# Optimization experiments

Measured on AMD Instinct MI355X. Metric: run time of the kernel, lower is better.

Reference implementation:

```python
import jax, jax.numpy as jnp
import numpy as np

B, S, DIM, H, D = 2, 2048, 1024, 16, 64
WINDOW = 512
MAX_MEM_SEGMENTS = 1
ROPE_THETA = 10000.0


def _rope(t, pos):
    # lucidrains rotary-embedding-torch default: interleaved pairs
    d = t.shape[-1]
    inv_freq = 1.0 / (ROPE_THETA ** (jnp.arange(0, d, 2, dtype=jnp.float32) / d))
    freqs = pos[:, None].astype(jnp.float32) * inv_freq[None, :]        # [S, d/2]
    freqs = jnp.repeat(freqs, 2, axis=-1)                               # [S, d]
    cos, sin = jnp.cos(freqs), jnp.sin(freqs)
    t1, t2 = t[..., 0::2], t[..., 1::2]
    rot = jnp.stack((-t2, t1), axis=-1).reshape(t.shape)                # rotate_half
    return t * cos + rot * sin


def setup_inputs() -> dict:
    key = jax.random.key(0)
    ks = jax.random.split(key, 8)
    tokens = jax.random.normal(ks[0], (B, S, DIM), dtype=jnp.float32)
    value_residual = jax.random.normal(ks[1], (B, H, S, D), dtype=jnp.float32)
    episode_ids = jnp.sort(jax.random.randint(ks[2], (B, S), 0, 4), axis=-1)
    w = 0.02
    Wq = jax.random.normal(ks[3], (DIM, H * D), dtype=jnp.float32) * w
    Wkv = jax.random.normal(ks[4], (DIM, 2 * H * D), dtype=jnp.float32) * w
    Wo = jax.random.normal(ks[5], (H * D, DIM), dtype=jnp.float32) * w
    Wg = jax.random.normal(ks[6], (DIM, H), dtype=jnp.float32) * w
    Wmix = jax.random.normal(ks[7], (DIM, H), dtype=jnp.float32) * w
    return {"tokens": tokens, "value_residual": value_residual, "episode_ids": episode_ids,
            "Wq": Wq, "Wkv": Wkv, "Wo": Wo, "Wg": Wg, "Wmix": Wmix}


def reference(tokens, value_residual, episode_ids, Wq, Wkv, Wo, Wg, Wmix):
    b, s, _ = tokens.shape
    scale = D ** -0.5

    def split_heads(x):  # [b, n, h*d] -> [b, h, n, d]
        return x.reshape(b, s, H, D).transpose(0, 2, 1, 3)

    q = split_heads(tokens @ Wq)
    kv = tokens @ Wkv
    k, v = split_heads(kv[..., :H * D]), split_heads(kv[..., H * D:])

    q = q * scale

    # value-residual lerp: v.lerp(value_residual, mix)
    mix = jax.nn.sigmoid(jnp.einsum('bnd,dh->bhn', tokens, Wmix))[..., None]  # [b,h,n,1]
    v = v + mix * (value_residual - v)

    pos = jnp.arange(s)
    q = _rope(q, pos)
    k = _rope(k, pos)

    sim = jnp.einsum('bhid,bhjd->bhij', q, k)

    # fixed-window causal mask: masked where dist < 0 or dist > max_mem_segments*window
    dist = pos[:, None] - pos[None, :]
    win_mask = (dist < 0) | (dist > MAX_MEM_SEGMENTS * WINDOW)            # [s, s]
    ep_mask = episode_ids[:, :, None] != episode_ids[:, None, :]          # [b, s, s]
    mask = win_mask[None, None, :, :] | ep_mask[:, None, :, :]

    sim = jnp.where(mask, -jnp.finfo(sim.dtype).max, sim)
    attn = jax.nn.softmax(sim, axis=-1)
    out = jnp.einsum('bhij,bhjd->bhid', attn, v)

    # sigmoid value gating
    gate = jax.nn.sigmoid(jnp.einsum('bnd,dh->bhn', tokens, Wg))[..., None]
    out = out * gate

    out = out.transpose(0, 2, 1, 3).reshape(b, s, H * D)
    return out @ Wo
```

## Files before the change

### kernel.cpp

```cpp
#include <hip/hip_runtime.h>
#include <math.h>

#define BB 2
#define SS 2048
#define DIMM 1024
#define HH 16
#define DD 64
#define WINDOW 512

typedef __bf16 bf16x8 __attribute__((ext_vector_type(8)));
typedef float f32x4 __attribute__((ext_vector_type(4)));

__device__ __forceinline__ unsigned short f2bf(float f) {
    unsigned int u = __float_as_uint(f);
    u = (u + 0x7FFFu + ((u >> 16) & 1u)) >> 16;
    return (unsigned short)u;
}
__device__ __forceinline__ float bf2f(unsigned short u) {
    return __uint_as_float((unsigned int)u << 16);
}

__device__ __forceinline__ void async_cp16(unsigned short* lds_dst, const unsigned short* g_src) {
    __builtin_amdgcn_global_load_lds(
        (const __attribute__((address_space(1))) unsigned int*)g_src,
        (__attribute__((address_space(3))) unsigned int*)lds_dst, 16, 0, 0);
}

__global__ __launch_bounds__(256) void cvt_bf16_kernel(
    const float* __restrict__ src, unsigned short* __restrict__ dst, int n4)
{
    for (int i = blockIdx.x * 256 + threadIdx.x; i < n4; i += gridDim.x * 256) {
        float4 v = ((const float4*)src)[i];
        ushort4 o;
        o.x = f2bf(v.x); o.y = f2bf(v.y); o.z = f2bf(v.z); o.w = f2bf(v.w);
        ((ushort4*)dst)[i] = o;
    }
}

__global__ __launch_bounds__(256) void transpose_cvt_kernel(
    const float* __restrict__ src, unsigned short* __restrict__ dst, int R, int C)
{
    __shared__ float t[32][33];
    int c0 = blockIdx.x * 32, r0 = blockIdx.y * 32;
    int tx = threadIdx.x, ty = threadIdx.y;
    #pragma unroll
    for (int u = 0; u < 4; ++u)
        t[ty + 8 * u][tx] = src[(size_t)(r0 + ty + 8 * u) * C + c0 + tx];
    __syncthreads();
    #pragma unroll
    for (int u = 0; u < 4; ++u)
        dst[(size_t)(c0 + ty + 8 * u) * R + r0 + tx] = f2bf(t[tx][ty + 8 * u]);
}

__global__ __launch_bounds__(256) void build_wgmt_kernel(
    const float* __restrict__ Wg, const float* __restrict__ Wmix,
    unsigned short* __restrict__ dst)
{
    int idx = blockIdx.x * 256 + threadIdx.x;
    int n = idx >> 10, k = idx & 1023;
    const float* src = (n < 16) ? Wg : Wmix;
    dst[idx] = f2bf(src[k * HH + (n & 15)]);
}

__global__ __launch_bounds__(256) void mixgate_mfma(
    const unsigned short* __restrict__ A,
    const unsigned short* __restrict__ Bt,
    float* __restrict__ gate, float* __restrict__ mix)
{
    int mbase = blockIdx.x * 32;
    int tid = threadIdx.x;
    int wave = tid >> 6, lane = tid & 63;
    int fr = lane & 15, hi = lane >> 4;
    int kw = wave * 256;

    __shared__ float red[4][32][32];

    f32x4 acc[2][2];
    #pragma unroll
    for (int m_ = 0; m_ < 2; ++m_)
        #pragma unroll
        for (int n_ = 0; n_ < 2; ++n_)
            acc[m_][n_] = (f32x4){0.f, 0.f, 0.f, 0.f};

    const unsigned short* a0 = A + (size_t)(mbase + fr) * 1024 + kw + hi * 8;
    const unsigned short* a1 = A + (size_t)(mbase + 16 + fr) * 1024 + kw + hi * 8;
    const unsigned short* b0 = Bt + (size_t)fr * 1024 + kw + hi * 8;
    const unsigned short* b1 = Bt + (size_t)(16 + fr) * 1024 + kw + hi * 8;

    #pragma unroll 2
    for (int k = 0; k < 256; k += 32) {
        bf16x8 af0 = *(const bf16x8*)(a0 + k);
        bf16x8 af1 = *(const bf16x8*)(a1 + k);
        bf16x8 bf0 = *(const bf16x8*)(b0 + k);
        bf16x8 bf1 = *(const bf16x8*)(b1 + k);
        acc[0][0] = __builtin_amdgcn_mfma_f32_16x16x32_bf16(af0, bf0, acc[0][0], 0, 0, 0);
        acc[0][1] = __builtin_amdgcn_mfma_f32_16x16x32_bf16(af0, bf1, acc[0][1], 0, 0, 0);
        acc[1][0] = __builtin_amdgcn_mfma_f32_16x16x32_bf16(af1, bf0, acc[1][0], 0, 0, 0);
        acc[1][1] = __builtin_amdgcn_mfma_f32_16x16x32_bf16(af1, bf1, acc[1][1], 0, 0, 0);
    }

    #pragma unroll
    for (int m_ = 0; m_ < 2; ++m_)
        #pragma unroll
        for (int n_ = 0; n_ < 2; ++n_)
            #pragma unroll
            for (int j = 0; j < 4; ++j)
                red[wave][m_ * 16 + hi * 4 + j][n_ * 16 + fr] = acc[m_][n_][j];
    __syncthreads();

    #pragma unroll
    for (int e = 0; e < 4; ++e) {
        int idx = (tid << 2) | e;
        int r = idx >> 5, c = idx & 31;
        float s4 = red[0][r][c] + red[1][r][c] + red[2][r][c] + red[3][r][c];
        float sg = 1.f / (1.f + __expf(-s4));
        int mg = mbase + r;
        int b = mg >> 11, s = mg & 2047;
        int h = c & 15;
        float* dst = (c < 16) ? gate : mix;
        dst[((size_t)b * HH + h) * SS + s] = sg;
    }
}

__global__ __launch_bounds__(256) void epstart_kernel(
    const int* __restrict__ ep, int* __restrict__ epstart)
{
    int idx = blockIdx.x * 256 + threadIdx.x;
    int b = idx >> 11, i = idx & 2047;
    const int* e = ep + b * SS;
    int v = e[i];
    int lo = 0, hi = i;
    while (lo < hi) {
        int mid = (lo + hi) >> 1;
        if (e[mid] == v) hi = mid; else lo = mid + 1;
    }
    epstart[idx] = lo;
}

template<int EPI>
__global__ __launch_bounds__(256) void gemm_mfma(
    const unsigned short* __restrict__ A, const unsigned short* __restrict__ Bt,
    void* __restrict__ o0v, void* __restrict__ o1v, void* __restrict__ o2v)
{
    const int K = 1024;
    int nbase = blockIdx.x * 128;
    int mbase = blockIdx.y * 128;
    int tid = threadIdx.x;
    int lane = tid & 63;
    int wave = tid >> 6;
    int wr = wave >> 1, wc = wave & 1;
    int fr = lane & 15, hi = lane >> 4;

    __shared__ unsigned short As[128 * 32];
    __shared__ unsigned short Bs[128 * 32];

    int srow = tid >> 2;
    int sp   = tid & 3;
    int scol = (sp ^ ((srow >> 1) & 3)) * 8;
    const unsigned short* agp0 = A  + (size_t)(mbase + srow) * K + scol;
    const unsigned short* agp1 = A  + (size_t)(mbase + srow + 64) * K + scol;
    const unsigned short* bgp0 = Bt + (size_t)(nbase + srow) * K + scol;
    const unsigned short* bgp1 = Bt + (size_t)(nbase + srow + 64) * K + scol;
    unsigned short* al0 = &As[tid * 8];
    unsigned short* al1 = &As[2048 + tid * 8];
    unsigned short* bl0 = &Bs[tid * 8];
    unsigned short* bl1 = &Bs[2048 + tid * 8];

    f32x4 acc[4][4];
    #pragma unroll
    for (int m_ = 0; m_ < 4; ++m_)
        #pragma unroll
        for (int n_ = 0; n_ < 4; ++n_)
            acc[m_][n_] = (f32x4){0.f, 0.f, 0.f, 0.f};

    int aidx[4], bidx[4];
    #pragma unroll
    for (int m_ = 0; m_ < 4; ++m_) {
        int row = wr * 64 + m_ * 16 + fr;
        aidx[m_] = row * 32 + (hi ^ ((row >> 1) & 3)) * 8;
    }
    #pragma unroll
    for (int n_ = 0; n_ < 4; ++n_) {
        int row = wc * 64 + n_ * 16 + fr;
        bidx[n_] = row * 32 + (hi ^ ((row >> 1) & 3)) * 8;
    }

    for (int k0 = 0; k0 < K; k0 += 32) {
        __syncthreads();
        async_cp16(al0, agp0 + k0);
        async_cp16(al1, agp1 + k0);
        async_cp16(bl0, bgp0 + k0);
        async_cp16(bl1, bgp1 + k0);
        __syncthreads();

        bf16x8 af[4], bfr[4];
        #pragma unroll
        for (int m_ = 0; m_ < 4; ++m_) af[m_] = *(const bf16x8*)&As[aidx[m_]];
        #pragma unroll
        for (int n_ = 0; n_ < 4; ++n_) bfr[n_] = *(const bf16x8*)&Bs[bidx[n_]];
        #pragma unroll
        for (int m_ = 0; m_ < 4; ++m_)
            #pragma unroll
            for (int n_ = 0; n_ < 4; ++n_)
                acc[m_][n_] = __builtin_amdgcn_mfma_f32_16x16x32_bf16(
                    af[m_], bfr[n_], acc[m_][n_], 0, 0, 0);
    }

    #pragma unroll
    for (int m_ = 0; m_ < 4; ++m_) {
        #pragma unroll
        for (int n_ = 0; n_ < 4; ++n_) {
            int c = nbase + wc * 64 + n_ * 16 + fr;
            #pragma unroll
            for (int j = 0; j < 4; ++j) {
                int mg = mbase + wr * 64 + m_ * 16 + hi * 4 + j;
                float v = acc[m_][n_][j];
                if (EPI == 0) {
                    ((float*)o0v)[(size_t)mg * 1024 + c] = v;
                } else {
                    int b = mg >> 11, s = mg & 2047;
                    int cc = c & 1023, h = cc >> 6, d = cc & 63;
                    unsigned short* dst = (c < 1024) ? (unsigned short*)o0v
                                        : (c < 2048) ? (unsigned short*)o1v
                                                     : (unsigned short*)o2v;
                    dst[(((size_t)b * HH + h) * SS + s) * DD + d] = f2bf(v);
                }
            }
        }
    }
}

__global__ __launch_bounds__(256) void rope_lerp_kernel(
    unsigned short* __restrict__ q, unsigned short* __restrict__ k,
    const unsigned short* __restrict__ v0, const float* __restrict__ vres,
    const float* __restrict__ mix, unsigned short* __restrict__ vt)
{
    int st = blockIdx.x;
    int bh = blockIdx.y;
    int tid = threadIdx.x;
    int sl = tid >> 2;
    int dg = (tid & 3) * 16;
    int s = st * 64 + sl;
    size_t rowoff = ((size_t)bh * SS + s) * DD + dg;

    __shared__ unsigned short vtile[64][66];

    union { uint4 v[2]; unsigned short u[16]; } qa, ka, va;
    qa.v[0] = *(const uint4*)(q + rowoff);
    qa.v[1] = *(const uint4*)(q + rowoff + 8);
    ka.v[0] = *(const uint4*)(k + rowoff);
    ka.v[1] = *(const uint4*)(k + rowoff + 8);
    va.v[0] = *(const uint4*)(v0 + rowoff);
    va.v[1] = *(const uint4*)(v0 + rowoff + 8);
    float4 w[4];
    #pragma unroll
    for (int u = 0; u < 4; ++u) w[u] = *(const float4*)(vres + rowoff + 4 * u);
    float mx = mix[(size_t)bh * SS + s];

    #pragma unroll
    for (int u = 0; u < 8; ++u) {
        int d0 = dg + 2 * u;
        float inv_freq = powf(10000.f, -(float)d0 * (1.f / 64.f));
        float fr = (float)s * inv_freq;
        float red = fr - 6.2831853f * floorf(fr * 0.15915494f);
        float cs, sn;
        __sincosf(red, &sn, &cs);
        float x = bf2f(qa.u[2 * u]), y = bf2f(qa.u[2 * u + 1]);
        qa.u[2 * u]     = f2bf((x * cs - y * sn) * 0.125f);
        qa.u[2 * u + 1] = f2bf((y * cs + x * sn) * 0.125f);
        x = bf2f(ka.u[2 * u]); y = bf2f(ka.u[2 * u + 1]);
        ka.u[2 * u]     = f2bf(x * cs - y * sn);
        ka.u[2 * u + 1] = f2bf(y * cs + x * sn);
    }
    *(uint4*)(q + rowoff)     = qa.v[0];
    *(uint4*)(q + rowoff + 8) = qa.v[1];
    *(uint4*)(k + rowoff)     = ka.v[0];
    *(uint4*)(k + rowoff + 8) = ka.v[1];

    #pragma unroll
    for (int e = 0; e < 16; ++e) {
        float vv = bf2f(va.u[e]);
        float wr = ((const float*)w)[e];
        vtile[sl][dg + e] = f2bf(vv + mx * (wr - vv));
    }
    __syncthreads();

    int d = tid >> 2;
    int sseg = (tid & 3) * 16;
    union { uint4 v[2]; unsigned short u[16]; } ot;
    #pragma unroll
    for (int e = 0; e < 16; ++e) ot.u[e] = vtile[sseg + e][d];
    unsigned short* dst = vt + ((size_t)bh * DD + d) * SS + st * 64 + sseg;
    *(uint4*)dst = ot.v[0];
    *(uint4*)(dst + 8) = ot.v[1];
}

__global__ __launch_bounds__(256) void attn_mfma(
    const unsigned short* __restrict__ qbh, const unsigned short* __restrict__ kbh,
    const unsigned short* __restrict__ vt, const int* __restrict__ epstart,
    const float* __restrict__ gate, unsigned short* __restrict__ ao)
{
    int orig = blockIdx.x;
    int swz  = (orig & 7) * 128 + (orig >> 3);
    int bh = swz >> 5, qt = swz & 31;
    int b = bh >> 4, h = bh & 15;
    int q0 = qt * 64;
    int tid = threadIdx.x;
    int wave = tid >> 6, lane = tid & 63;
    int lq = lane & 15, lg = lane >> 4;
    int i = q0 + wave * 16 + lq;

    __shared__ unsigned short Ks[4096];
    __shared__ unsigned short Vs[4096];
    alignas(16) __shared__ unsigned short P_lds[4][16][72];

    int srow0 = tid >> 3, sch = tid & 7;
    int srow1 = srow0 + 32;
    int sc0 = ((sch ^ (srow0 & 7)) << 3);
    int sc1 = ((sch ^ (srow1 & 7)) << 3);
    const unsigned short* kS0 = kbh + ((size_t)bh * SS + srow0) * DD + sc0;
    const unsigned short* kS1 = kbh + ((size_t)bh * SS + srow1) * DD + sc1;
    const unsigned short* vS0 = vt + ((size_t)bh * DD + srow0) * SS + sc0;
    const unsigned short* vS1 = vt + ((size_t)bh * DD + srow1) * SS + sc1;
    unsigned short* kd0 = &Ks[tid * 8];
    unsigned short* kd1 = &Ks[2048 + tid * 8];
    unsigned short* vd0 = &Vs[tid * 8];
    unsigned short* vd1 = &Vs[2048 + tid * 8];

    int fidx[4];
    #pragma unroll
    for (int n = 0; n < 4; ++n) {
        int r = 16 * n + lq;
        fidx[n] = r * 64 + ((lg ^ (r & 7)) << 3);
    }

    const unsigned short* qrow = qbh + ((size_t)bh * SS + i) * DD + lg * 8;
    bf16x8 bq0 = *(const bf16x8*)qrow;
    bf16x8 bq1 = *(const bf16x8*)(qrow + 32);

    int jmin = i - WINDOW;
    int es = epstart[b * SS + i];
    if (es > jmin) jmin = es;
    float gi = gate[(size_t)bh * SS + i];

    float m = -1e30f, l = 0.f;
    f32x4 o[4];
    #pragma unroll
    for (int n = 0; n < 4; ++n) o[n] = (f32x4){0.f, 0.f, 0.f, 0.f};

    int t0 = (qt < 8) ? (8 - qt) : 0;
    for (int t = t0; t < 9; ++t) {
        int jbase = 64 * (qt - 8 + t);

        __syncthreads();
        async_cp16(kd0, kS0 + (size_t)jbase * DD);
        async_cp16(kd1, kS1 + (size_t)jbase * DD);
        async_cp16(vd0, vS0 + jbase);
        async_cp16(vd1, vS1 + jbase);
        __syncthreads();

        f32x4 acc[4];
        #pragma unroll
        for (int n = 0; n < 4; ++n) acc[n] = (f32x4){0.f, 0.f, 0.f, 0.f};
        #pragma unroll
        for (int n = 0; n < 4; ++n) {
            bf16x8 kf0 = *(const bf16x8*)&Ks[fidx[n]];
            bf16x8 kf1 = *(const bf16x8*)&Ks[fidx[n] ^ 32];
            acc[n] = __builtin_amdgcn_mfma_f32_16x16x32_bf16(kf0, bq0, acc[n], 0, 0, 0);
            acc[n] = __builtin_amdgcn_mfma_f32_16x16x32_bf16(kf1, bq1, acc[n], 0, 0, 0);
        }

        int jb = jbase + lg * 4;
        #pragma unroll
        for (int n = 0; n < 4; ++n)
            #pragma unroll
            for (int r = 0; r < 4; ++r) {
                int j = jb + 16 * n + r;
                if (j < jmin || j > i) acc[n][r] = -3e38f;
            }

        float tm = -3e38f;
        #pragma unroll
        for (int n = 0; n < 4; ++n)
            tm = fmaxf(tm, fmaxf(fmaxf(acc[n][0], acc[n][1]), fmaxf(acc[n][2], acc[n][3])));
        tm = fmaxf(tm, __shfl_xor(tm, 16, 64));
        tm = fmaxf(tm, __shfl_xor(tm, 32, 64));
        float mnew = fmaxf(m, tm);
        float scale = __expf(m - mnew);
        float ts = 0.f;
        #pragma unroll
        for (int n = 0; n < 4; ++n)
            #pragma unroll
            for (int r = 0; r < 4; ++r) {
                float p = __expf(acc[n][r] - mnew);
                acc[n][r] = p;
                ts += p;
            }
        ts += __shfl_xor(ts, 16, 64);
        ts += __shfl_xor(ts, 32, 64);
        l = l * scale + ts;
        m = mnew;
        #pragma unroll
        for (int n = 0; n < 4; ++n) o[n] = o[n] * scale;

        #pragma unroll
        for (int n = 0; n < 4; ++n) {
            ushort4 u;
            u.x = f2bf(acc[n][0]); u.y = f2bf(acc[n][1]);
            u.z = f2bf(acc[n][2]); u.w = f2bf(acc[n][3]);
            *(ushort4*)&P_lds[wave][lq][16 * n + lg * 4] = u;
        }
        bf16x8 bp0 = *(const bf16x8*)&P_lds[wave][lq][lg * 8];
        bf16x8 bp1 = *(const bf16x8*)&P_lds[wave][lq][32 + lg * 8];

        #pragma unroll
        for (int n = 0; n < 4; ++n) {
            bf16x8 vf0 = *(const bf16x8*)&Vs[fidx[n]];
            bf16x8 vf1 = *(const bf16x8*)&Vs[fidx[n] ^ 32];
            o[n] = __builtin_amdgcn_mfma_f32_16x16x32_bf16(vf0, bp0, o[n], 0, 0, 0);
            o[n] = __builtin_amdgcn_mfma_f32_16x16x32_bf16(vf1, bp1, o[n], 0, 0, 0);
        }
    }

    float g = gi / l;
    #pragma unroll
    for (int n = 0; n < 4; ++n) {
        ushort4 u;
        u.x = f2bf(o[n][0] * g); u.y = f2bf(o[n][1] * g);
        u.z = f2bf(o[n][2] * g); u.w = f2bf(o[n][3] * g);
        *(ushort4*)(ao + (((size_t)b * SS + i) * HH + h) * DD + 16 * n + lg * 4) = u;
    }
}

extern "C" void kernel_launch(void* const* d_in, const int* in_sizes, int n_in,
                              void* d_out, int out_size, void* d_ws, size_t ws_size,
                              hipStream_t stream)
{
    const float* tokens = (const float*)d_in[0];
    const float* vres   = (const float*)d_in[1];
    const int*   ep     = (const int*)d_in[2];
    const float* Wq     = (const float*)d_in[3];
    const float* Wkv    = (const float*)d_in[4];
    const float* Wo     = (const float*)d_in[5];
    const float* Wg     = (const float*)d_in[6];
    const float* Wmix   = (const float*)d_in[7];
    float* out = (float*)d_out;

    char* wsb = (char*)d_ws;
    unsigned short* qbh  = (unsigned short*)(wsb + 0);
    unsigned short* kbh  = (unsigned short*)(wsb + 8388608);
    unsigned short* vb0  = (unsigned short*)(wsb + 16777216);
    unsigned short* vtb  = (unsigned short*)(wsb + 25165824);
    unsigned short* aob  = (unsigned short*)(wsb + 33554432);
    unsigned short* tokA = (unsigned short*)(wsb + 41943040);
    unsigned short* BtW  = (unsigned short*)(wsb + 50331648);
    unsigned short* WotW = BtW;
    float* gatep = (float*)(wsb + 56623104);
    float* mixp  = (float*)(wsb + 56885248);
    int*   epst  = (int*)(wsb + 57147392);
    unsigned short* wgmt = (unsigned short*)(wsb + 57163776);

    cvt_bf16_kernel<<<2048, 256, 0, stream>>>(tokens, tokA, (BB * SS * DIMM) / 4);
    transpose_cvt_kernel<<<dim3(32, 32), dim3(32, 8), 0, stream>>>(Wq,  BtW,               1024, 1024);
    transpose_cvt_kernel<<<dim3(64, 32), dim3(32, 8), 0, stream>>>(Wkv, BtW + 1024 * 1024, 1024, 2048);
    build_wgmt_kernel<<<128, 256, 0, stream>>>(Wg, Wmix, wgmt);
    epstart_kernel<<<16, 256, 0, stream>>>(ep, epst);

    mixgate_mfma<<<128, 256, 0, stream>>>(tokA, wgmt, gatep, mixp);
    gemm_mfma<1><<<dim3(24, 32), 256, 0, stream>>>(tokA, BtW, qbh, kbh, vb0);
    rope_lerp_kernel<<<dim3(SS / 64, BB * HH), 256, 0, stream>>>(qbh, kbh, vb0, vres, mixp, vtb);
    attn_mfma<<<1024, 256, 0, stream>>>(qbh, kbh, vtb, epst, gatep, aob);

    transpose_cvt_kernel<<<dim3(32, 32), dim3(32, 8), 0, stream>>>(Wo, WotW, 1024, 1024);
    gemm_mfma<0><<<dim3(8, 32), 256, 0, stream>>>(aob, WotW, out, nullptr, nullptr);
}
```

Before: 132.1 us.

## Double-buffer LDS staging in GEMM and use narrower N tile for output projection

The bf16 MFMA GEMM now keeps two LDS buffers and issues the async global-to-LDS copy for the next K slice before computing on the current one. This removes one barrier per iteration and is meant to overlap global loads with MFMA work. The tile width in N becomes a template parameter, and the output projection drops to 64 columns so it launches 512 blocks instead of 256, which should fill the CUs better. The cost is double the LDS per block. Correctness now depends on the async copies being complete and visible before the next barrier.

```diff
diff --git a/kernel.cpp b/kernel.cpp
--- a/kernel.cpp
+++ b/kernel.cpp
@@ -137,13 +137,14 @@
     epstart[idx] = lo;
 }
 
-template<int EPI>
+template<int EPI, int BN>
 __global__ __launch_bounds__(256) void gemm_mfma(
     const unsigned short* __restrict__ A, const unsigned short* __restrict__ Bt,
     void* __restrict__ o0v, void* __restrict__ o1v, void* __restrict__ o2v)
 {
     const int K = 1024;
-    int nbase = blockIdx.x * 128;
+    constexpr int NFR = BN / 32;
+    int nbase = blockIdx.x * BN;
     int mbase = blockIdx.y * 128;
     int tid = threadIdx.x;
     int lane = tid & 63;
@@ -151,8 +152,8 @@
     int wr = wave >> 1, wc = wave & 1;
     int fr = lane & 15, hi = lane >> 4;
 
-    __shared__ unsigned short As[128 * 32];
-    __shared__ unsigned short Bs[128 * 32];
+    __shared__ unsigned short As[2][128 * 32];
+    __shared__ unsigned short Bs[2][BN * 32];
 
     int srow = tid >> 2;
     int sp   = tid & 3;
@@ -160,48 +161,51 @@
     const unsigned short* agp0 = A  + (size_t)(mbase + srow) * K + scol;
     const unsigned short* agp1 = A  + (size_t)(mbase + srow + 64) * K + scol;
     const unsigned short* bgp0 = Bt + (size_t)(nbase + srow) * K + scol;
-    const unsigned short* bgp1 = Bt + (size_t)(nbase + srow + 64) * K + scol;
-    unsigned short* al0 = &As[tid * 8];
-    unsigned short* al1 = &As[2048 + tid * 8];
-    unsigned short* bl0 = &Bs[tid * 8];
-    unsigned short* bl1 = &Bs[2048 + tid * 8];
-
-    f32x4 acc[4][4];
+    const unsigned short* bgp1 = (BN == 128)
+        ? Bt + (size_t)(nbase + srow + 64) * K + scol : bgp0;
+
+    f32x4 acc[4][NFR];
     #pragma unroll
     for (int m_ = 0; m_ < 4; ++m_)
         #pragma unroll
-        for (int n_ = 0; n_ < 4; ++n_)
+        for (int n_ = 0; n_ < NFR; ++n_)
             acc[m_][n_] = (f32x4){0.f, 0.f, 0.f, 0.f};
 
-    int aidx[4], bidx[4];
+    int aidx[4], bidx[NFR];
     #pragma unroll
     for (int m_ = 0; m_ < 4; ++m_) {
         int row = wr * 64 + m_ * 16 + fr;
         aidx[m_] = row * 32 + (hi ^ ((row >> 1) & 3)) * 8;
     }
     #pragma unroll
-    for (int n_ = 0; n_ < 4; ++n_) {
-        int row = wc * 64 + n_ * 16 + fr;
+    for (int n_ = 0; n_ < NFR; ++n_) {
+        int row = wc * (BN / 2) + n_ * 16 + fr;
         bidx[n_] = row * 32 + (hi ^ ((row >> 1) & 3)) * 8;
     }
 
+    auto stage = [&](int buf, int k0) {
+        async_cp16(&As[buf][tid * 8], agp0 + k0);
+        async_cp16(&As[buf][2048 + tid * 8], agp1 + k0);
+        async_cp16(&Bs[buf][tid * 8], bgp0 + k0);
+        if constexpr (BN == 128)
+            async_cp16(&Bs[buf][2048 + tid * 8], bgp1 + k0);
+    };
+
+    stage(0, 0);
     for (int k0 = 0; k0 < K; k0 += 32) {
+        int cur = (k0 >> 5) & 1;
         __syncthreads();
-        async_cp16(al0, agp0 + k0);
-        async_cp16(al1, agp1 + k0);
-        async_cp16(bl0, bgp0 + k0);
-        async_cp16(bl1, bgp1 + k0);
-        __syncthreads();
-
-        bf16x8 af[4], bfr[4];
-        #pragma unroll
-        for (int m_ = 0; m_ < 4; ++m_) af[m_] = *(const bf16x8*)&As[aidx[m_]];
-        #pragma unroll
-        for (int n_ = 0; n_ < 4; ++n_) bfr[n_] = *(const bf16x8*)&Bs[bidx[n_]];
+        if (k0 + 32 < K) stage(cur ^ 1, k0 + 32);
+
+        bf16x8 af[4], bfr[NFR];
+        #pragma unroll
+        for (int m_ = 0; m_ < 4; ++m_) af[m_] = *(const bf16x8*)&As[cur][aidx[m_]];
+        #pragma unroll
+        for (int n_ = 0; n_ < NFR; ++n_) bfr[n_] = *(const bf16x8*)&Bs[cur][bidx[n_]];
         #pragma unroll
         for (int m_ = 0; m_ < 4; ++m_)
             #pragma unroll
-            for (int n_ = 0; n_ < 4; ++n_)
+            for (int n_ = 0; n_ < NFR; ++n_)
                 acc[m_][n_] = __builtin_amdgcn_mfma_f32_16x16x32_bf16(
                     af[m_], bfr[n_], acc[m_][n_], 0, 0, 0);
     }
@@ -209,8 +213,8 @@
     #pragma unroll
     for (int m_ = 0; m_ < 4; ++m_) {
         #pragma unroll
-        for (int n_ = 0; n_ < 4; ++n_) {
-            int c = nbase + wc * 64 + n_ * 16 + fr;
+        for (int n_ = 0; n_ < NFR; ++n_) {
+            int c = nbase + wc * (BN / 2) + n_ * 16 + fr;
             #pragma unroll
             for (int j = 0; j < 4; ++j) {
                 int mg = mbase + wr * 64 + m_ * 16 + hi * 4 + j;
@@ -467,10 +471,10 @@
     epstart_kernel<<<16, 256, 0, stream>>>(ep, epst);
 
     mixgate_mfma<<<128, 256, 0, stream>>>(tokA, wgmt, gatep, mixp);
-    gemm_mfma<1><<<dim3(24, 32), 256, 0, stream>>>(tokA, BtW, qbh, kbh, vb0);
+    gemm_mfma<1, 128><<<dim3(24, 32), 256, 0, stream>>>(tokA, BtW, qbh, kbh, vb0);
     rope_lerp_kernel<<<dim3(SS / 64, BB * HH), 256, 0, stream>>>(qbh, kbh, vb0, vres, mixp, vtb);
     attn_mfma<<<1024, 256, 0, stream>>>(qbh, kbh, vtb, epst, gatep, aob);
 
     transpose_cvt_kernel<<<dim3(32, 32), dim3(32, 8), 0, stream>>>(Wo, WotW, 1024, 1024);
-    gemm_mfma<0><<<dim3(8, 32), 256, 0, stream>>>(aob, WotW, out, nullptr, nullptr);
-}
+    gemm_mfma<0, 64><<<dim3(16, 32), 256, 0, stream>>>(aob, WotW, out, nullptr, nullptr);
+}
```

Result: faster. 128.0 us (-3.1%).
